# Kernel optimization log

Measured on AMD Instinct MI355X. Metric: run time of the kernel, lower is better.

The kernel has to match this reference:

```python
import jax, jax.numpy as jnp
import numpy as np

N_NODES = 100000
N_EDGES = 1600000
IN_F = 256
OUT_F = 128


def setup_inputs() -> dict:
    key = jax.random.key(0)
    k1, k2, k3, k4, k5, k6 = jax.random.split(key, 6)
    x = jax.random.normal(k1, (N_NODES, IN_F), dtype=jnp.float32)
    edge_src = jax.random.randint(k2, (N_EDGES,), 0, N_NODES, dtype=jnp.int64)
    edge_dst = jax.random.randint(k3, (N_EDGES,), 0, N_NODES, dtype=jnp.int64)
    edge_weight = jax.random.uniform(k4, (N_EDGES,), dtype=jnp.float32)
    stdv = 1.0 / np.sqrt(OUT_F)
    w = jax.random.uniform(k5, (IN_F, OUT_F), dtype=jnp.float32, minval=-stdv, maxval=stdv)
    b = jax.random.uniform(k6, (OUT_F,), dtype=jnp.float32, minval=-stdv, maxval=stdv)
    return {"x": x, "edge_src": edge_src, "edge_dst": edge_dst,
            "edge_weight": edge_weight, "w": w, "b": b}


def reference(x, edge_src, edge_dst, edge_weight, w, b):
    # dense feature transform: [N, in] @ [in, out] -> [N, out]
    h = x @ w
    # sparse adjacency SpMM: out[i] = sum_{e: dst[e]==i} a[e] * h[src[e]]
    msgs = h[edge_src] * edge_weight[:, None]          # [E, out]
    agg = jax.ops.segment_sum(msgs, edge_dst, num_segments=N_NODES)
    return agg + b
```

## Files before the change

### kernel.cpp

```cpp
#include <hip/hip_runtime.h>

#define N_NODES 100000
#define N_EDGES 1600000
#define IN_F 256
#define OUT_F 128

#define NBUCK 1563
#define NCH   500
#define CH    3200
#define BCAP  2048
#define SCAP  256

typedef __attribute__((ext_vector_type(8))) short bf16x8;
typedef __attribute__((ext_vector_type(4))) float f32x4;

static __device__ __forceinline__ unsigned f2bf_u(float f) {
    unsigned u = __float_as_uint(f);
    return (u + 0x7FFFu + ((u >> 16) & 1u)) >> 16;
}
static __device__ __forceinline__ float bf2f(short s) {
    return __uint_as_float(((unsigned)(unsigned short)s) << 16);
}
static __device__ __forceinline__ bf16x8 pack_bf16x8(float4 a, float4 b) {
    union { unsigned u[4]; bf16x8 v; } r;
    r.u[0] = f2bf_u(a.x) | (f2bf_u(a.y) << 16);
    r.u[1] = f2bf_u(a.z) | (f2bf_u(a.w) << 16);
    r.u[2] = f2bf_u(b.x) | (f2bf_u(b.y) << 16);
    r.u[3] = f2bf_u(b.z) | (f2bf_u(b.w) << 16);
    return r.v;
}

__global__ __launch_bounds__(1024) void init_kernel(int* __restrict__ gadd,
                                                    const float* __restrict__ w,
                                                    unsigned short* __restrict__ wtf) {
    const int t = threadIdx.x;
    if (blockIdx.x == 0) {
        for (int i = t; i < 8 * NBUCK; i += 1024) gadd[i] = 0;
        return;
    }
    const int id = (blockIdx.x - 1) * 1024 + t;
    const int f = id >> 6, lane = id & 63;
    const int ks = f >> 3, nt = f & 7;
    const int m = lane & 15, q = lane >> 4;
    const int row = nt * 16 + m;
    const int col0 = ks * 32 + q * 8;
    unsigned short* o = wtf + (size_t)f * 512 + lane * 8;
    #pragma unroll
    for (int j = 0; j < 8; ++j)
        o[j] = (unsigned short)f2bf_u(w[(size_t)(col0 + j) * OUT_F + row]);
}

__global__ __launch_bounds__(1024) void part_kernel(const int* __restrict__ edge_src,
                                                    const int* __restrict__ edge_dst,
                                                    const float* __restrict__ edge_weight,
                                                    int* __restrict__ gadd,
                                                    int2* __restrict__ part) {
    __shared__ int h[NBUCK];
    const int t = threadIdx.x;
    const int c = blockIdx.x;
    const int stripe = c & 7;
    const int sbase = stripe << 8;
    for (int i = t; i < NBUCK; i += 1024) h[i] = 0;
    __syncthreads();

    const int e0 = c * CH;
    const int4*   d4 = (const int4*)(edge_dst + e0);
    const int4*   s4 = (const int4*)(edge_src + e0);
    const float4* w4 = (const float4*)(edge_weight + e0);

    int4   dd, ss;
    float4 ww;
    const bool val = (t < CH / 4);
    if (val) {
        dd = d4[t];
        ss = s4[t];
        ww = w4[t];
        atomicAdd(&h[dd.x >> 6], 1);
        atomicAdd(&h[dd.y >> 6], 1);
        atomicAdd(&h[dd.z >> 6], 1);
        atomicAdd(&h[dd.w >> 6], 1);
    }
    __syncthreads();

    int* g = gadd + stripe * NBUCK;
    for (int i = t; i < NBUCK; i += 1024) {
        const int cnt = h[i];
        int base = 0;
        if (cnt > 0) base = atomicAdd(&g[i], cnt);
        h[i] = (i << 11) + sbase + base;
    }
    __syncthreads();

    if (val) {
        int b, pos;
        b = dd.x >> 6; pos = atomicAdd(&h[b], 1);
        if (pos < (b << 11) + sbase + SCAP)
            part[pos] = make_int2(ss.x | ((dd.x & 63) << 24), __float_as_int(ww.x));
        b = dd.y >> 6; pos = atomicAdd(&h[b], 1);
        if (pos < (b << 11) + sbase + SCAP)
            part[pos] = make_int2(ss.y | ((dd.y & 63) << 24), __float_as_int(ww.y));
        b = dd.z >> 6; pos = atomicAdd(&h[b], 1);
        if (pos < (b << 11) + sbase + SCAP)
            part[pos] = make_int2(ss.z | ((dd.z & 63) << 24), __float_as_int(ww.z));
        b = dd.w >> 6; pos = atomicAdd(&h[b], 1);
        if (pos < (b << 11) + sbase + SCAP)
            part[pos] = make_int2(ss.w | ((dd.w & 63) << 24), __float_as_int(ww.w));
    }
}

__global__ __launch_bounds__(1024, 8) void gemm_mfma_kernel(const float* __restrict__ x,
                                                            const unsigned short* __restrict__ wtf,
                                                            unsigned short* __restrict__ hb) {
    __shared__ unsigned short bs[64 * 512];
    const int t = threadIdx.x;

    {
        const uint4* wsrc = (const uint4*)wtf;
        uint4* wdst = (uint4*)bs;
        #pragma unroll
        for (int i = 0; i < 4; ++i) wdst[t + i * 1024] = wsrc[t + i * 1024];
    }
    __syncthreads();

    const int wave = t >> 6, lane = t & 63;
    const int m = lane & 15, quad = lane >> 4;
    const int row0 = blockIdx.x * 256 + wave * 16;

    int r = row0 + m; if (r >= N_NODES) r = N_NODES - 1;
    const float4* xr = (const float4*)(x + (size_t)r * IN_F) + quad * 2;

    f32x4 acc[8];
    #pragma unroll
    for (int nt = 0; nt < 8; ++nt) acc[nt] = (f32x4){0.f, 0.f, 0.f, 0.f};

    const bf16x8* bfrag = (const bf16x8*)bs;
    #pragma unroll
    for (int ks = 0; ks < 8; ++ks) {
        const bf16x8 a = pack_bf16x8(xr[ks * 8], xr[ks * 8 + 1]);
        #pragma unroll
        for (int nt = 0; nt < 8; ++nt) {
            const bf16x8 bf = bfrag[(ks * 8 + nt) * 64 + lane];
            acc[nt] = __builtin_amdgcn_mfma_f32_16x16x32_bf16(a, bf, acc[nt], 0, 0, 0);
        }
    }

    #pragma unroll
    for (int nt = 0; nt < 8; ++nt) {
        #pragma unroll
        for (int rr = 0; rr < 4; ++rr) {
            const int orow = row0 + quad * 4 + rr;
            if (orow < N_NODES)
                hb[(size_t)orow * OUT_F + nt * 16 + m] = (unsigned short)f2bf_u(acc[nt][rr]);
        }
    }
}

__global__ __launch_bounds__(512) void spmm_kernel(const unsigned short* __restrict__ hb,
                                                   const int* __restrict__ gadd,
                                                   const int2* __restrict__ part,
                                                   const float* __restrict__ b,
                                                   float* __restrict__ out) {
    __shared__ int lh[64];
    __shared__ int lstart[65];
    __shared__ int lcur[64];
    __shared__ int cs[8];
    __shared__ int csum[9];
    __shared__ int2 list[BCAP];

    const int t = threadIdx.x;
    const int bucket = blockIdx.x;
    const int base = bucket * 64;

    if (t < 64) lh[t] = 0;
    if (t < 8) {
        int cc = gadd[t * NBUCK + bucket];
        cs[t] = cc > SCAP ? SCAP : cc;
    }
    __syncthreads();
    if (t == 0) {
        int a = 0;
        csum[0] = 0;
        #pragma unroll
        for (int i = 0; i < 8; ++i) { a += cs[i]; csum[i + 1] = a; }
    }
    __syncthreads();
    const int total = csum[8];

    int2 stash[4];
    int  sn[4];
    #pragma unroll
    for (int sub = 0; sub < 4; ++sub) {
        const int idx = sub * 512 + t;
        sn[sub] = -1;
        if (idx < total) {
            int sdx = 0;
            #pragma unroll
            for (int q = 1; q < 8; ++q) sdx += (idx >= csum[q]);
            const int local = idx - csum[sdx];
            const int2 en = part[((size_t)bucket << 11) + (sdx << 8) + local];
            const int n = ((unsigned)en.x) >> 24;
            sn[sub] = n;
            stash[sub] = make_int2(en.x & 0xFFFFFF, en.y);
            atomicAdd(&lh[n], 1);
        }
    }
    __syncthreads();

    if (t < 64) {
        const int v = lh[t];
        int s = v;
        #pragma unroll
        for (int off = 1; off < 64; off <<= 1) {
            const int o = __shfl_up(s, off);
            if (t >= off) s += o;
        }
        lstart[t] = s - v;
        lcur[t]   = s - v;
        if (t == 63) lstart[64] = s;
    }
    __syncthreads();

    #pragma unroll
    for (int sub = 0; sub < 4; ++sub) {
        if (sn[sub] >= 0) {
            const int pos = atomicAdd(&lcur[sn[sub]], 1);
            list[pos] = stash[sub];
        }
    }
    __syncthreads();

    const int j = t & 15;
    const float4* b4 = (const float4*)b;
    const float4 bb0 = b4[j * 2];
    const float4 bb1 = b4[j * 2 + 1];

    #pragma unroll
    for (int g = 0; g < 2; ++g) {
        const int n = g * 32 + (t >> 4);
        const int node = base + n;
        if (node >= N_NODES) continue;
        float4 acc0 = bb0, acc1 = bb1;
        int p = lstart[n];
        const int p1 = lstart[n + 1];
        for (; p + 4 <= p1; p += 4) {
            const int2 sw0 = list[p];
            const int2 sw1 = list[p + 1];
            const int2 sw2 = list[p + 2];
            const int2 sw3 = list[p + 3];
            const bf16x8 h0 = *(const bf16x8*)(hb + (size_t)sw0.x * OUT_F + j * 8);
            const bf16x8 h1 = *(const bf16x8*)(hb + (size_t)sw1.x * OUT_F + j * 8);
            const bf16x8 h2 = *(const bf16x8*)(hb + (size_t)sw2.x * OUT_F + j * 8);
            const bf16x8 h3 = *(const bf16x8*)(hb + (size_t)sw3.x * OUT_F + j * 8);
            const float w0 = __int_as_float(sw0.y);
            const float w1 = __int_as_float(sw1.y);
            const float w2 = __int_as_float(sw2.y);
            const float w3 = __int_as_float(sw3.y);
            acc0.x += w0 * bf2f(h0[0]); acc0.y += w0 * bf2f(h0[1]);
            acc0.z += w0 * bf2f(h0[2]); acc0.w += w0 * bf2f(h0[3]);
            acc1.x += w0 * bf2f(h0[4]); acc1.y += w0 * bf2f(h0[5]);
            acc1.z += w0 * bf2f(h0[6]); acc1.w += w0 * bf2f(h0[7]);
            acc0.x += w1 * bf2f(h1[0]); acc0.y += w1 * bf2f(h1[1]);
            acc0.z += w1 * bf2f(h1[2]); acc0.w += w1 * bf2f(h1[3]);
            acc1.x += w1 * bf2f(h1[4]); acc1.y += w1 * bf2f(h1[5]);
            acc1.z += w1 * bf2f(h1[6]); acc1.w += w1 * bf2f(h1[7]);
            acc0.x += w2 * bf2f(h2[0]); acc0.y += w2 * bf2f(h2[1]);
            acc0.z += w2 * bf2f(h2[2]); acc0.w += w2 * bf2f(h2[3]);
            acc1.x += w2 * bf2f(h2[4]); acc1.y += w2 * bf2f(h2[5]);
            acc1.z += w2 * bf2f(h2[6]); acc1.w += w2 * bf2f(h2[7]);
            acc0.x += w3 * bf2f(h3[0]); acc0.y += w3 * bf2f(h3[1]);
            acc0.z += w3 * bf2f(h3[2]); acc0.w += w3 * bf2f(h3[3]);
            acc1.x += w3 * bf2f(h3[4]); acc1.y += w3 * bf2f(h3[5]);
            acc1.z += w3 * bf2f(h3[6]); acc1.w += w3 * bf2f(h3[7]);
        }
        for (; p < p1; ++p) {
            const int2 sw = list[p];
            const float wgt = __int_as_float(sw.y);
            const bf16x8 hv = *(const bf16x8*)(hb + (size_t)sw.x * OUT_F + j * 8);
            acc0.x += wgt * bf2f(hv[0]); acc0.y += wgt * bf2f(hv[1]);
            acc0.z += wgt * bf2f(hv[2]); acc0.w += wgt * bf2f(hv[3]);
            acc1.x += wgt * bf2f(hv[4]); acc1.y += wgt * bf2f(hv[5]);
            acc1.z += wgt * bf2f(hv[6]); acc1.w += wgt * bf2f(hv[7]);
        }
        float4* o4 = (float4*)(out + (size_t)node * OUT_F + j * 8);
        o4[0] = acc0;
        o4[1] = acc1;
    }
}

extern "C" void kernel_launch(void* const* d_in, const int* in_sizes, int n_in,
                              void* d_out, int out_size, void* d_ws, size_t ws_size,
                              hipStream_t stream) {
    const float* x           = (const float*)d_in[0];
    const int*   edge_src    = (const int*)d_in[1];
    const int*   edge_dst    = (const int*)d_in[2];
    const float* edge_weight = (const float*)d_in[3];
    const float* w           = (const float*)d_in[4];
    const float* b           = (const float*)d_in[5];
    float* out = (float*)d_out;

    char* ws = (char*)d_ws;
    size_t off = 0;
    unsigned short* hb  = (unsigned short*)(ws + off);
    off += (size_t)N_NODES * OUT_F * 2;           off = (off + 15) & ~(size_t)15;
    unsigned short* wtf = (unsigned short*)(ws + off);
    off += (size_t)IN_F * OUT_F * 2;              off = (off + 15) & ~(size_t)15;
    int* gadd = (int*)(ws + off);
    off += (size_t)8 * NBUCK * 4;                 off = (off + 15) & ~(size_t)15;
    int2* part = (int2*)(ws + off);
    off += (size_t)NBUCK * BCAP * 8;

    init_kernel<<<5, 1024, 0, stream>>>(gadd, w, wtf);
    part_kernel<<<NCH, 1024, 0, stream>>>(edge_src, edge_dst, edge_weight, gadd, part);
    gemm_mfma_kernel<<<(N_NODES + 255) / 256, 1024, 0, stream>>>(x, wtf, hb);
    spmm_kernel<<<NBUCK, 512, 0, stream>>>(hb, gadd, part, b, out);
}
```

Baseline: 269.9 us.

## Fuse edge partitioning and MFMA GEMM into one interleaved launch

Merges the edge bucketing kernel and the bf16 MFMA feature-transform GEMM into a single launch. Blocks are interleaved in groups of 16, with the first 8 doing partition chunks and the last 8 doing GEMM tiles, and the two roles share LDS through a union. The aim is to overlap the atomic-heavy, memory-bound partition pass with the GEMM and to save one launch and its tail. The cost is a larger shared footprint for the partition blocks and some early-exiting idle blocks.

```diff
diff --git a/kernel.cpp b/kernel.cpp
--- a/kernel.cpp
+++ b/kernel.cpp
@@ -10,6 +10,8 @@
 #define CH    3200
 #define BCAP  2048
 #define SCAP  256
+#define NTILE 391
+#define NFUSE 1008
 
 typedef __attribute__((ext_vector_type(8))) short bf16x8;
 typedef __attribute__((ext_vector_type(4))) float f32x4;
@@ -50,73 +52,83 @@
         o[j] = (unsigned short)f2bf_u(w[(size_t)(col0 + j) * OUT_F + row]);
 }
 
-__global__ __launch_bounds__(1024) void part_kernel(const int* __restrict__ edge_src,
-                                                    const int* __restrict__ edge_dst,
-                                                    const float* __restrict__ edge_weight,
-                                                    int* __restrict__ gadd,
-                                                    int2* __restrict__ part) {
-    __shared__ int h[NBUCK];
+union SMem {
+    int h[NBUCK];
+    unsigned short bs[64 * 512];
+};
+
+__global__ __launch_bounds__(1024, 8) void fused_kernel(const int* __restrict__ edge_src,
+                                                        const int* __restrict__ edge_dst,
+                                                        const float* __restrict__ edge_weight,
+                                                        int* __restrict__ gadd,
+                                                        int2* __restrict__ part,
+                                                        const float* __restrict__ x,
+                                                        const unsigned short* __restrict__ wtf,
+                                                        unsigned short* __restrict__ hb) {
+    __shared__ SMem sm;
     const int t = threadIdx.x;
-    const int c = blockIdx.x;
-    const int stripe = c & 7;
-    const int sbase = stripe << 8;
-    for (int i = t; i < NBUCK; i += 1024) h[i] = 0;
-    __syncthreads();
-
-    const int e0 = c * CH;
-    const int4*   d4 = (const int4*)(edge_dst + e0);
-    const int4*   s4 = (const int4*)(edge_src + e0);
-    const float4* w4 = (const float4*)(edge_weight + e0);
-
-    int4   dd, ss;
-    float4 ww;
-    const bool val = (t < CH / 4);
-    if (val) {
-        dd = d4[t];
-        ss = s4[t];
-        ww = w4[t];
-        atomicAdd(&h[dd.x >> 6], 1);
-        atomicAdd(&h[dd.y >> 6], 1);
-        atomicAdd(&h[dd.z >> 6], 1);
-        atomicAdd(&h[dd.w >> 6], 1);
-    }
-    __syncthreads();
-
-    int* g = gadd + stripe * NBUCK;
-    for (int i = t; i < NBUCK; i += 1024) {
-        const int cnt = h[i];
-        int base = 0;
-        if (cnt > 0) base = atomicAdd(&g[i], cnt);
-        h[i] = (i << 11) + sbase + base;
-    }
-    __syncthreads();
-
-    if (val) {
-        int b, pos;
-        b = dd.x >> 6; pos = atomicAdd(&h[b], 1);
-        if (pos < (b << 11) + sbase + SCAP)
-            part[pos] = make_int2(ss.x | ((dd.x & 63) << 24), __float_as_int(ww.x));
-        b = dd.y >> 6; pos = atomicAdd(&h[b], 1);
-        if (pos < (b << 11) + sbase + SCAP)
-            part[pos] = make_int2(ss.y | ((dd.y & 63) << 24), __float_as_int(ww.y));
-        b = dd.z >> 6; pos = atomicAdd(&h[b], 1);
-        if (pos < (b << 11) + sbase + SCAP)
-            part[pos] = make_int2(ss.z | ((dd.z & 63) << 24), __float_as_int(ww.z));
-        b = dd.w >> 6; pos = atomicAdd(&h[b], 1);
-        if (pos < (b << 11) + sbase + SCAP)
-            part[pos] = make_int2(ss.w | ((dd.w & 63) << 24), __float_as_int(ww.w));
-    }
-}
-
-__global__ __launch_bounds__(1024, 8) void gemm_mfma_kernel(const float* __restrict__ x,
-                                                            const unsigned short* __restrict__ wtf,
-                                                            unsigned short* __restrict__ hb) {
-    __shared__ unsigned short bs[64 * 512];
-    const int t = threadIdx.x;
+    const int group = blockIdx.x >> 4, within = blockIdx.x & 15;
+
+    if (within < 8) {
+        const int c = group * 8 + within;
+        if (c >= NCH) return;
+        const int stripe = within;
+        const int sbase = stripe << 8;
+        for (int i = t; i < NBUCK; i += 1024) sm.h[i] = 0;
+        __syncthreads();
+
+        const int e0 = c * CH;
+        const int4*   d4 = (const int4*)(edge_dst + e0);
+        const int4*   s4 = (const int4*)(edge_src + e0);
+        const float4* w4 = (const float4*)(edge_weight + e0);
+
+        int4   dd, ss;
+        float4 ww;
+        const bool val = (t < CH / 4);
+        if (val) {
+            dd = d4[t];
+            ss = s4[t];
+            ww = w4[t];
+            atomicAdd(&sm.h[dd.x >> 6], 1);
+            atomicAdd(&sm.h[dd.y >> 6], 1);
+            atomicAdd(&sm.h[dd.z >> 6], 1);
+            atomicAdd(&sm.h[dd.w >> 6], 1);
+        }
+        __syncthreads();
+
+        int* g = gadd + stripe * NBUCK;
+        for (int i = t; i < NBUCK; i += 1024) {
+            const int cnt = sm.h[i];
+            int base = 0;
+            if (cnt > 0) base = atomicAdd(&g[i], cnt);
+            sm.h[i] = (i << 11) + sbase + base;
+        }
+        __syncthreads();
+
+        if (val) {
+            int b, pos;
+            b = dd.x >> 6; pos = atomicAdd(&sm.h[b], 1);
+            if (pos < (b << 11) + sbase + SCAP)
+                part[pos] = make_int2(ss.x | ((dd.x & 63) << 24), __float_as_int(ww.x));
+            b = dd.y >> 6; pos = atomicAdd(&sm.h[b], 1);
+            if (pos < (b << 11) + sbase + SCAP)
+                part[pos] = make_int2(ss.y | ((dd.y & 63) << 24), __float_as_int(ww.y));
+            b = dd.z >> 6; pos = atomicAdd(&sm.h[b], 1);
+            if (pos < (b << 11) + sbase + SCAP)
+                part[pos] = make_int2(ss.z | ((dd.z & 63) << 24), __float_as_int(ww.z));
+            b = dd.w >> 6; pos = atomicAdd(&sm.h[b], 1);
+            if (pos < (b << 11) + sbase + SCAP)
+                part[pos] = make_int2(ss.w | ((dd.w & 63) << 24), __float_as_int(ww.w));
+        }
+        return;
+    }
+
+    const int tile = group * 8 + (within - 8);
+    if (tile >= NTILE) return;
 
     {
         const uint4* wsrc = (const uint4*)wtf;
-        uint4* wdst = (uint4*)bs;
+        uint4* wdst = (uint4*)sm.bs;
         #pragma unroll
         for (int i = 0; i < 4; ++i) wdst[t + i * 1024] = wsrc[t + i * 1024];
     }
@@ -124,7 +136,7 @@
 
     const int wave = t >> 6, lane = t & 63;
     const int m = lane & 15, quad = lane >> 4;
-    const int row0 = blockIdx.x * 256 + wave * 16;
+    const int row0 = tile * 256 + wave * 16;
 
     int r = row0 + m; if (r >= N_NODES) r = N_NODES - 1;
     const float4* xr = (const float4*)(x + (size_t)r * IN_F) + quad * 2;
@@ -133,7 +145,7 @@
     #pragma unroll
     for (int nt = 0; nt < 8; ++nt) acc[nt] = (f32x4){0.f, 0.f, 0.f, 0.f};
 
-    const bf16x8* bfrag = (const bf16x8*)bs;
+    const bf16x8* bfrag = (const bf16x8*)sm.bs;
     #pragma unroll
     for (int ks = 0; ks < 8; ++ks) {
         const bf16x8 a = pack_bf16x8(xr[ks * 8], xr[ks * 8 + 1]);
@@ -310,7 +322,7 @@
     off += (size_t)NBUCK * BCAP * 8;
 
     init_kernel<<<5, 1024, 0, stream>>>(gadd, w, wtf);
-    part_kernel<<<NCH, 1024, 0, stream>>>(edge_src, edge_dst, edge_weight, gadd, part);
-    gemm_mfma_kernel<<<(N_NODES + 255) / 256, 1024, 0, stream>>>(x, wtf, hb);
+    fused_kernel<<<NFUSE, 1024, 0, stream>>>(edge_src, edge_dst, edge_weight, gadd, part,
+                                             x, wtf, hb);
     spmm_kernel<<<NBUCK, 512, 0, stream>>>(hb, gadd, part, b, out);
 }
```

After: 275.4 us. 1.02x slower.
